# Kernel tuning notes

Measured on AMD Instinct MI355X. Metric: run time of the kernel, lower is better.

The kernel has to match this reference:

```python
import jax, jax.numpy as jnp
import numpy as np

B, D, H, E, K = 8192, 1024, 4096, 8, 2
LOSS_COEF = 0.01
EPS_COMBINE = float(np.finfo(np.float64).eps)  # np.finfo(float).eps used in combine


def setup_inputs() -> dict:
    key = jax.random.key(0)
    ks = jax.random.split(key, 6)
    s_in = 1.0 / np.sqrt(D)
    s_hid = 1.0 / np.sqrt(H)
    return {
        "x": jax.random.normal(ks[0], (B, D), jnp.float32),
        "w_gate": jax.random.uniform(ks[1], (E, D), jnp.float32, -s_in, s_in),
        "fc1_w": jax.random.uniform(ks[2], (E, H, D), jnp.float32, -s_in, s_in),
        "fc1_b": jax.random.uniform(ks[3], (E, H), jnp.float32, -s_in, s_in),
        "fc2_w": jax.random.uniform(ks[4], (E, D, H), jnp.float32, -s_hid, s_hid),
        "fc2_b": jax.random.uniform(ks[5], (E, D), jnp.float32, -s_hid, s_hid),
    }


def _cv_squared(v):
    # torch .var() uses ddof=1
    return jnp.var(v, ddof=1) / (jnp.mean(v) ** 2 + 1e-10)


def _top_k_gating(x, w_gate):
    # clean logits (noisy_gating=False): [B, E]
    logits = x @ w_gate.T
    top_vals, top_idx = jax.lax.top_k(logits, K + 1)  # min(k+1, E)
    topk_vals = top_vals[:, :K]
    topk_idx = top_idx[:, :K]
    topk_gates = jax.nn.softmax(topk_vals, axis=1)
    gates = jnp.zeros((x.shape[0], E), x.dtype)
    gates = gates.at[jnp.arange(x.shape[0])[:, None], topk_idx].set(topk_gates)
    return gates


def _forward(x, w_gate, fc1_w, fc1_b, fc2_w, fc2_b):
    gates = _top_k_gating(x, w_gate)            # [B, E], sparse (k nonzeros/row)
    importance = gates.sum(axis=0)              # [E]
    load = (gates > 0).sum(axis=0).astype(jnp.float32)
    loss = (_cv_squared(importance) + _cv_squared(load)) * LOSS_COEF

    # Dense-equivalent expert compute: tokens with gate==0 contribute 0 to the
    # combine, identical math to SparseDispatcher's gather/scatter.
    h = jnp.einsum('bd,ehd->beh', x, fc1_w) + fc1_b            # [B, E, H]
    h = jax.nn.gelu(h, approximate=False)                      # torch exact gelu
    o = jnp.einsum('beh,edh->bed', h, fc2_w) + fc2_b           # [B, E, D]
    log_p = jax.nn.log_softmax(o, axis=-1)                     # LogSoftmax(dim=1)

    # combine: exp, weight by gates, scatter-add, eps-fill, log
    combined = jnp.einsum('be,bed->bd', gates, jnp.exp(log_p)) # [B, D]
    combined = jnp.where(combined == 0, EPS_COMBINE, combined)
    y = jnp.log(combined)
    return y, loss


def reference(x, w_gate, fc1_w, fc1_b, fc2_w, fc2_b):
    return _forward(x, w_gate, fc1_w, fc1_b, fc2_w, fc2_b)
```

## Files before the change

### kernel.cpp

```cpp
#include <hip/hip_runtime.h>
#include <cstdint>
#include <cmath>

#define BT 8192
#define DD 1024
#define HH 4096
#define EE 8
#define MT2 72

typedef __attribute__((ext_vector_type(8))) short short8;
typedef __attribute__((ext_vector_type(4))) float f32x4;
typedef unsigned short u16;
typedef unsigned int u32;

__device__ __forceinline__ u16 f2bf(float f) {
    u32 u = __float_as_uint(f);
    u += 0x7FFFu + ((u >> 16) & 1u);
    return (u16)(u >> 16);
}

__device__ __forceinline__ void gld_lds16(const void* g, void* l) {
    __builtin_amdgcn_global_load_lds((__attribute__((address_space(1))) void*)g,
                                     (__attribute__((address_space(3))) void*)l,
                                     16, 0, 0);
}

__global__ void cvt_kernel(const float* __restrict__ src, u16* __restrict__ dst, int n8) {
    int i = blockIdx.x * blockDim.x + threadIdx.x;
    if (i >= n8) return;
    size_t base = (size_t)i * 8;
    float4 a = *(const float4*)(src + base);
    float4 b = *(const float4*)(src + base + 4);
    uint4 o;
    o.x = (u32)f2bf(a.x) | ((u32)f2bf(a.y) << 16);
    o.y = (u32)f2bf(a.z) | ((u32)f2bf(a.w) << 16);
    o.z = (u32)f2bf(b.x) | ((u32)f2bf(b.y) << 16);
    o.w = (u32)f2bf(b.z) | ((u32)f2bf(b.w) << 16);
    *(uint4*)(dst + base) = o;
}

__global__ void gating_kernel(const float* __restrict__ x, const float* __restrict__ wg,
                              float* __restrict__ gate_arr, int* __restrict__ list,
                              int* __restrict__ info,
                              int* __restrict__ counts, float* __restrict__ importance) {
    int wave = (blockIdx.x * blockDim.x + threadIdx.x) >> 6;
    int lane = threadIdx.x & 63;
    if (wave >= BT) return;
    const float* xr = x + (size_t)wave * DD;
    double acc[EE];
#pragma unroll
    for (int e = 0; e < EE; ++e) acc[e] = 0.0;
#pragma unroll
    for (int c = 0; c < DD / 256; ++c) {
        const int i = c * 256 + lane * 4;
        float4 xv = *(const float4*)(xr + i);
        double x0 = xv.x, x1 = xv.y, x2 = xv.z, x3 = xv.w;
#pragma unroll
        for (int e = 0; e < EE; ++e) {
            float4 wv = *(const float4*)(wg + e * DD + i);
            acc[e] += x0 * (double)wv.x + x1 * (double)wv.y
                    + x2 * (double)wv.z + x3 * (double)wv.w;
        }
    }
#pragma unroll
    for (int e = 0; e < EE; ++e) {
        double v = acc[e];
        for (int off = 32; off; off >>= 1) v += __shfl_down(v, off, 64);
        acc[e] = v;
    }
    if (lane == 0) {
        int i0 = 0; double v0 = acc[0];
        for (int e = 1; e < EE; ++e) if (acc[e] > v0) { v0 = acc[e]; i0 = e; }
        int i1 = -1; double v1 = -1e300;
        for (int e = 0; e < EE; ++e) { if (e == i0) continue; if (acc[e] > v1) { v1 = acc[e]; i1 = e; } }
        double e1 = exp(v1 - v0);
        double s = 1.0 + e1;
        float g0 = (float)(1.0 / s);
        float g1 = (float)(e1 / s);
        gate_arr[2 * wave]     = g0;
        gate_arr[2 * wave + 1] = g1;
        atomicAdd(&importance[i0], g0);
        atomicAdd(&importance[i1], g1);
        int p0 = atomicAdd(&counts[i0], 1);
        list[i0 * BT + p0] = wave;
        int p1 = atomicAdd(&counts[i1], 1);
        list[i1 * BT + p1] = wave;
        info[2 * wave]     = (i0 << 16) | p0;
        info[2 * wave + 1] = (i1 << 16) | p1;
    }
}

__global__ void loss_kernel(const int* __restrict__ counts, const float* __restrict__ importance,
                            int* __restrict__ offs, float* __restrict__ out_loss,
                            int* __restrict__ tmap, int* __restrict__ ntiles) {
    if (threadIdx.x == 0 && blockIdx.x == 0) {
        double mi = 0, ml = 0;
        int off = 0;
        for (int e = 0; e < EE; e++) {
            offs[e] = off; off += counts[e];
            mi += (double)importance[e]; ml += (double)counts[e];
        }
        mi /= EE; ml /= EE;
        double vi = 0, vl = 0;
        for (int e = 0; e < EE; e++) {
            double di = (double)importance[e] - mi; vi += di * di;
            double dl = (double)counts[e] - ml;     vl += dl * dl;
        }
        vi /= (EE - 1); vl /= (EE - 1);
        double cv_i = vi / (mi * mi + 1e-10);
        double cv_l = vl / (ml * ml + 1e-10);
        *out_loss = (float)((cv_i + cv_l) * 0.01);
        int ntl = 0;
        for (int e = 0; e < EE; e++)
            for (int t = 0; t < counts[e]; t += 256)
                tmap[ntl++] = (e << 20) | t;
        *ntiles = ntl;
    }
}

__global__ void gather_x_kernel(const float* __restrict__ x, const int* __restrict__ list,
                                const int* __restrict__ counts, const int* __restrict__ offs,
                                u16* __restrict__ xg) {
    int r = blockIdx.x;
    int e = 0;
#pragma unroll
    for (int i = 1; i < EE; ++i) if (r >= offs[i]) e = i;
    int m = r - offs[e];
    if (m >= counts[e]) return;
    int token = list[e * BT + m];
    const float* src = x + (size_t)token * DD;
    u16* dst = xg + (size_t)r * DD;
    int i = threadIdx.x * 4;
    float4 a = *(const float4*)(src + i);
    uint2 o;
    o.x = (u32)f2bf(a.x) | ((u32)f2bf(a.y) << 16);
    o.y = (u32)f2bf(a.z) | ((u32)f2bf(a.w) << 16);
    *(uint2*)(dst + i) = o;
}

template <int K, int NT, bool GELU, bool GATHER>
__global__ __launch_bounds__(512) void moe_gemm(const u16* __restrict__ Asrc,
                                                const u16* __restrict__ Bsrc,
                                                const float* __restrict__ bias,
                                                const int* __restrict__ list,
                                                const int* __restrict__ counts,
                                                const int* __restrict__ offs,
                                                const int* __restrict__ tmap,
                                                const int* __restrict__ ntiles,
                                                u16* __restrict__ outB,
                                                float* __restrict__ outF) {
    constexpr int NXT = NT / 256;
    constexpr int nwg = NXT * MT2;
    constexpr int QW = nwg / 8;
    constexpr int ITERS = K / 128;
    const int tid = threadIdx.x;
    const int lane = tid & 63;
    const int wv = tid >> 6;
    const int wqr = wv >> 2;
    const int wqc = wv & 3;
    const int kq = lane >> 4;
    const int rsub = lane & 15;
    const int rq = kq * 4;
    const int ks1 = tid >> 7;
    const int r128 = tid & 127;

    __shared__ u16 Ls[2][2][2][8192];

    const int nw = *ntiles;

#define STAGE_A(db, h, T)                                                   \
    do {                                                                    \
        gld_lds16(aP##h + (T) * 64,      &Ls[db][0][h][tid * 8]);           \
        gld_lds16(aP##h + (T) * 64 + 32, &Ls[db][0][h][(tid + 512) * 8]);   \
    } while (0)
#define STAGE_B(db, h, T)                                                   \
    do {                                                                    \
        gld_lds16(bP##h + (T) * 64,      &Ls[db][1][h][tid * 8]);           \
        gld_lds16(bP##h + (T) * 64 + 32, &Ls[db][1][h][(tid + 512) * 8]);   \
    } while (0)
#define WAIT4 asm volatile("s_waitcnt vmcnt(4)" ::: "memory")
#define WAIT0 asm volatile("s_waitcnt vmcnt(0)" ::: "memory")
#define NOOP ((void)0)

#define PH(db, mh, nh, RDA, STG, WT)                                          \
    do {                                                                      \
        if (RDA) {                                                            \
            _Pragma("unroll") for (int kk = 0; kk < 2; kk++)                  \
            _Pragma("unroll") for (int mi = 0; mi < 4; mi++)                  \
                afr[mi][kk] = *(const short8*)&Ls[db][0][mh]                  \
                    [((kk * 4 + kq) * 128 + wqr * 64 + mi * 16 + rsub) * 8];  \
        }                                                                     \
        _Pragma("unroll") for (int kk = 0; kk < 2; kk++)                      \
        _Pragma("unroll") for (int ni = 0; ni < 2; ni++)                      \
            bfr[ni][kk] = *(const short8*)&Ls[db][1][nh]                      \
                [((kk * 4 + kq) * 128 + wqc * 32 + ni * 16 + rsub) * 8];      \
        STG;                                                                  \
        __builtin_amdgcn_s_barrier();                                         \
        __builtin_amdgcn_s_setprio(1);                                        \
        _Pragma("unroll") for (int mi = 0; mi < 4; mi++)                      \
        _Pragma("unroll") for (int ni = 0; ni < 2; ni++)                      \
        _Pragma("unroll") for (int kk = 0; kk < 2; kk++)                      \
            acc[mh][nh][mi][ni] = __builtin_amdgcn_mfma_f32_16x16x32_bf16(    \
                afr[mi][kk], bfr[ni][kk], acc[mh][nh][mi][ni], 0, 0, 0);      \
        __builtin_amdgcn_s_setprio(0);                                        \
        WT;                                                                   \
        __builtin_amdgcn_s_barrier();                                         \
    } while (0)

#pragma unroll 1
    for (int raw = blockIdx.x; raw < nwg; raw += 256) {
        const int wg = (raw & 7) * QW + (raw >> 3);
        const int nt = wg / MT2;
        const int mt = wg - nt * MT2;
        if (mt >= nw) continue;
        const int ent = tmap[mt];
        const int e = ent >> 20;
        const int mbase = ent & 0xFFFFF;
        const int mmax = counts[e] - mbase;
        const int rowbase = offs[e] + mbase;
        const int nbase = nt * 256;

        size_t arow0, arow1;
        if constexpr (GATHER) {
            arow0 = (size_t)list[e * BT + mbase + min(r128, mmax - 1)];
            arow1 = (size_t)list[e * BT + mbase + min(128 + r128, mmax - 1)];
        } else {
            arow0 = (size_t)(rowbase + min(r128, mmax - 1));
            arow1 = (size_t)(rowbase + min(128 + r128, mmax - 1));
        }
        const u16* aP0 = Asrc + arow0 * (size_t)K + ks1 * 8;
        const u16* aP1 = Asrc + arow1 * (size_t)K + ks1 * 8;
        const u16* bP0 = Bsrc + ((size_t)e * NT + nbase + r128) * (size_t)K + ks1 * 8;
        const u16* bP1 = bP0 + (size_t)128 * K;

        f32x4 acc[2][2][4][2] = {};
        short8 afr[4][2], bfr[2][2];

        STAGE_A(0, 0, 0); STAGE_B(0, 0, 0); STAGE_A(0, 1, 0); STAGE_B(0, 1, 0);
        STAGE_A(1, 0, 1); STAGE_B(1, 0, 1);
        WAIT4;
        __builtin_amdgcn_s_barrier();

#pragma unroll 1
        for (int it = 0; it < ITERS - 1; ++it) {
            const int t = 2 * it;
            PH(0, 0, 0, 1, STAGE_A(1, 1, t + 1), NOOP);
            PH(0, 0, 1, 0, STAGE_B(1, 1, t + 1), NOOP);
            PH(0, 1, 0, 1, STAGE_A(0, 0, t + 2), NOOP);
            PH(0, 1, 1, 0, STAGE_B(0, 0, t + 2), WAIT4);
            PH(1, 0, 0, 1, STAGE_A(0, 1, t + 2), NOOP);
            PH(1, 0, 1, 0, STAGE_B(0, 1, t + 2), NOOP);
            PH(1, 1, 0, 1, STAGE_A(1, 0, t + 3), NOOP);
            PH(1, 1, 1, 0, STAGE_B(1, 0, t + 3), WAIT4);
        }
        {
            const int t = 2 * (ITERS - 1);
            PH(0, 0, 0, 1, STAGE_A(1, 1, t + 1), NOOP);
            PH(0, 0, 1, 0, STAGE_B(1, 1, t + 1), NOOP);
            PH(0, 1, 0, 1, NOOP, NOOP);
            PH(0, 1, 1, 0, NOOP, WAIT0);
            PH(1, 0, 0, 1, NOOP, NOOP);
            PH(1, 0, 1, 0, NOOP, NOOP);
            PH(1, 1, 0, 1, NOOP, NOOP);
            PH(1, 1, 1, 0, NOOP, NOOP);
        }

        float bvals[2][2];
#pragma unroll
        for (int nh = 0; nh < 2; nh++)
#pragma unroll
            for (int ni = 0; ni < 2; ni++)
                bvals[nh][ni] = bias[(size_t)e * NT + nbase + nh * 128 + wqc * 32 + ni * 16 + rsub];
#pragma unroll
        for (int mh = 0; mh < 2; mh++) {
#pragma unroll
            for (int mi = 0; mi < 4; mi++) {
#pragma unroll
                for (int r = 0; r < 4; r++) {
                    int m = mh * 128 + wqr * 64 + mi * 16 + rq + r;
                    if (m < mmax) {
                        size_t ro = (size_t)(rowbase + m);
#pragma unroll
                        for (int nh = 0; nh < 2; nh++) {
#pragma unroll
                            for (int ni = 0; ni < 2; ni++) {
                                int n = nbase + nh * 128 + wqc * 32 + ni * 16 + rsub;
                                float v = acc[mh][nh][mi][ni][r] + bvals[nh][ni];
                                if constexpr (GELU) {
                                    v = 0.5f * v * (1.0f + erff(v * 0.7071067811865476f));
                                    outB[ro * NT + n] = f2bf(v);
                                } else {
                                    outF[ro * NT + n] = v;
                                }
                            }
                        }
                    }
                }
            }
        }
        WAIT0;
    }
#undef PH
#undef STAGE_A
#undef STAGE_B
#undef WAIT4
#undef WAIT0
#undef NOOP
}

__global__ void combine_kernel(const float* __restrict__ o, const float* __restrict__ gates,
                               const int* __restrict__ info, const int* __restrict__ offs,
                               float* __restrict__ y) {
    const int b = blockIdx.x;
    const int tid = threadIdx.x;
    const int lane = tid & 63, wv = tid >> 6;
    const int inf0 = info[2 * b], inf1 = info[2 * b + 1];
    const int r0i = offs[inf0 >> 16] + (inf0 & 0xffff);
    const int r1i = offs[inf1 >> 16] + (inf1 & 0xffff);
    const float* r0 = o + (size_t)r0i * DD;
    const float* r1 = o + (size_t)r1i * DD;
    float v0[4], v1[4];
#pragma unroll
    for (int j = 0; j < 4; j++) { v0[j] = r0[tid + 256 * j]; v1[j] = r1[tid + 256 * j]; }
    float m0 = fmaxf(fmaxf(v0[0], v0[1]), fmaxf(v0[2], v0[3]));
    float m1 = fmaxf(fmaxf(v1[0], v1[1]), fmaxf(v1[2], v1[3]));
#pragma unroll
    for (int off = 32; off; off >>= 1) {
        m0 = fmaxf(m0, __shfl_xor(m0, off, 64));
        m1 = fmaxf(m1, __shfl_xor(m1, off, 64));
    }
    __shared__ float sred[2][4];
    if (lane == 0) { sred[0][wv] = m0; sred[1][wv] = m1; }
    __syncthreads();
    m0 = fmaxf(fmaxf(sred[0][0], sred[0][1]), fmaxf(sred[0][2], sred[0][3]));
    m1 = fmaxf(fmaxf(sred[1][0], sred[1][1]), fmaxf(sred[1][2], sred[1][3]));
    float p0[4], p1[4], s0 = 0.f, s1 = 0.f;
#pragma unroll
    for (int j = 0; j < 4; j++) {
        p0[j] = expf(v0[j] - m0); s0 += p0[j];
        p1[j] = expf(v1[j] - m1); s1 += p1[j];
    }
#pragma unroll
    for (int off = 32; off; off >>= 1) {
        s0 += __shfl_xor(s0, off, 64);
        s1 += __shfl_xor(s1, off, 64);
    }
    __shared__ float sred2[2][4];
    if (lane == 0) { sred2[0][wv] = s0; sred2[1][wv] = s1; }
    __syncthreads();
    s0 = sred2[0][0] + sred2[0][1] + sred2[0][2] + sred2[0][3];
    s1 = sred2[1][0] + sred2[1][1] + sred2[1][2] + sred2[1][3];
    const float c0 = gates[2 * b] / s0;
    const float c1 = gates[2 * b + 1] / s1;
#pragma unroll
    for (int j = 0; j < 4; j++) {
        float c = p0[j] * c0 + p1[j] * c1;
        if (c == 0.f) c = 2.2204460492503131e-16f;
        y[(size_t)b * DD + tid + 256 * j] = logf(c);
    }
}

extern "C" void kernel_launch(void* const* d_in, const int* in_sizes, int n_in,
                              void* d_out, int out_size, void* d_ws, size_t ws_size,
                              hipStream_t stream) {
    const float* x     = (const float*)d_in[0];
    const float* wgate = (const float*)d_in[1];
    const float* fc1w  = (const float*)d_in[2];
    const float* fc1b  = (const float*)d_in[3];
    const float* fc2w  = (const float*)d_in[4];
    const float* fc2b  = (const float*)d_in[5];
    float* out = (float*)d_out;

    char* ws = (char*)d_ws;
    const size_t MB = 1024 * 1024;
    const bool big = ws_size >= 289 * MB;
    u16* w1b = (u16*)(ws);
    float* o = (float*)(ws);
    u16* w2b = (u16*)(ws + 64 * MB);
    u16* xb  = (u16*)(ws + 128 * MB);
    u16* h   = (u16*)(ws + (big ? 128 : 144) * MB);
    u16* xg  = (u16*)(ws + 256 * MB);
    char* meta = ws + (big ? 288 : 272) * MB;
    int* counts       = (int*)meta;
    int* offs         = (int*)(meta + 32);
    float* importance = (float*)(meta + 64);
    int* ntiles       = (int*)(meta + 96);
    float* gate_arr   = (float*)(meta + 128);
    int* info         = (int*)(meta + 128 + 65536);
    int* list         = (int*)(meta + 128 + 131072);
    int* tmap         = (int*)(meta + 512 * 1024);

    hipMemsetAsync(meta, 0, 96, stream);
    cvt_kernel<<<(EE * HH * DD / 8 + 255) / 256, 256, 0, stream>>>(fc1w, w1b, EE * HH * DD / 8);
    cvt_kernel<<<(EE * DD * HH / 8 + 255) / 256, 256, 0, stream>>>(fc2w, w2b, EE * DD * HH / 8);
    gating_kernel<<<BT / 4, 256, 0, stream>>>(x, wgate, gate_arr, list, info, counts, importance);
    loss_kernel<<<1, 64, 0, stream>>>(counts, importance, offs, out + (size_t)BT * DD, tmap, ntiles);

    if (big) {
        gather_x_kernel<<<2 * BT, 256, 0, stream>>>(x, list, counts, offs, xg);
        moe_gemm<DD, HH, true, false><<<256, 512, 0, stream>>>(
            xg, w1b, fc1b, nullptr, counts, offs, tmap, ntiles, h, nullptr);
    } else {
        cvt_kernel<<<(BT * DD / 8 + 255) / 256, 256, 0, stream>>>(x, xb, BT * DD / 8);
        moe_gemm<DD, HH, true, true><<<256, 512, 0, stream>>>(
            xb, w1b, fc1b, list, counts, offs, tmap, ntiles, h, nullptr);
    }
    moe_gemm<HH, DD, false, false><<<256, 512, 0, stream>>>(
        h, w2b, fc2b, nullptr, counts, offs, tmap, ntiles, nullptr, o);
    combine_kernel<<<BT, 256, 0, stream>>>(o, gate_arr, info, offs, out);
}
```

Baseline: 1.150 ms.

## Software-pipeline LDS fragment reads one phase ahead of MFMA in grouped GEMM

Restructures the GEMM main loop so A/B fragment reads from LDS are double-buffered in registers and issued one phase ahead of the MFMA block that consumes them. Each phase now has one barrier instead of two, and the wait depth changes from vmcnt(4) to vmcnt(2), with extra barriers around the waits. The aim is to hide LDS read latency behind matrix-core work and cut barrier count. In exchange it needs more fragment registers, which could reduce occupancy, and the changed buffer-reuse ordering risks races if a read overlaps a stage write.

```diff
diff --git a/kernel.cpp b/kernel.cpp
--- a/kernel.cpp
+++ b/kernel.cpp
@@ -179,32 +179,33 @@
         gld_lds16(bP##h + (T) * 64 + 32, &Ls[db][1][h][(tid + 512) * 8]);   \
     } while (0)
 #define WAIT4 asm volatile("s_waitcnt vmcnt(4)" ::: "memory")
+#define WAIT2 asm volatile("s_waitcnt vmcnt(2)" ::: "memory")
 #define WAIT0 asm volatile("s_waitcnt vmcnt(0)" ::: "memory")
-#define NOOP ((void)0)
-
-#define PH(db, mh, nh, RDA, STG, WT)                                          \
+#define BAR __builtin_amdgcn_s_barrier()
+
+#define READ_A(s, db, mh)                                                     \
     do {                                                                      \
-        if (RDA) {                                                            \
-            _Pragma("unroll") for (int kk = 0; kk < 2; kk++)                  \
-            _Pragma("unroll") for (int mi = 0; mi < 4; mi++)                  \
-                afr[mi][kk] = *(const short8*)&Ls[db][0][mh]                  \
-                    [((kk * 4 + kq) * 128 + wqr * 64 + mi * 16 + rsub) * 8];  \
-        }                                                                     \
+        _Pragma("unroll") for (int kk = 0; kk < 2; kk++)                      \
+        _Pragma("unroll") for (int mi = 0; mi < 4; mi++)                      \
+            afr[s][mi][kk] = *(const short8*)&Ls[db][0][mh]                   \
+                [((kk * 4 + kq) * 128 + wqr * 64 + mi * 16 + rsub) * 8];      \
+    } while (0)
+#define READ_B(nh, db)                                                        \
+    do {                                                                      \
         _Pragma("unroll") for (int kk = 0; kk < 2; kk++)                      \
         _Pragma("unroll") for (int ni = 0; ni < 2; ni++)                      \
-            bfr[ni][kk] = *(const short8*)&Ls[db][1][nh]                      \
+            bfr[nh][ni][kk] = *(const short8*)&Ls[db][1][nh]                  \
                 [((kk * 4 + kq) * 128 + wqc * 32 + ni * 16 + rsub) * 8];      \
-        STG;                                                                  \
-        __builtin_amdgcn_s_barrier();                                         \
+    } while (0)
+#define MFMAQ(s, mh, nh)                                                      \
+    do {                                                                      \
         __builtin_amdgcn_s_setprio(1);                                        \
         _Pragma("unroll") for (int mi = 0; mi < 4; mi++)                      \
         _Pragma("unroll") for (int ni = 0; ni < 2; ni++)                      \
         _Pragma("unroll") for (int kk = 0; kk < 2; kk++)                      \
             acc[mh][nh][mi][ni] = __builtin_amdgcn_mfma_f32_16x16x32_bf16(    \
-                afr[mi][kk], bfr[ni][kk], acc[mh][nh][mi][ni], 0, 0, 0);      \
+                afr[s][mi][kk], bfr[nh][ni][kk], acc[mh][nh][mi][ni], 0, 0, 0);\
         __builtin_amdgcn_s_setprio(0);                                        \
-        WT;                                                                   \
-        __builtin_amdgcn_s_barrier();                                         \
     } while (0)
 
 #pragma unroll 1
@@ -234,35 +235,44 @@
         const u16* bP1 = bP0 + (size_t)128 * K;
 
         f32x4 acc[2][2][4][2] = {};
-        short8 afr[4][2], bfr[2][2];
+        short8 afr[2][4][2];
+        short8 bfr[2][2][2];
 
         STAGE_A(0, 0, 0); STAGE_B(0, 0, 0); STAGE_A(0, 1, 0); STAGE_B(0, 1, 0);
         STAGE_A(1, 0, 1); STAGE_B(1, 0, 1);
         WAIT4;
-        __builtin_amdgcn_s_barrier();
+        BAR;
+        READ_A(0, 0, 0);
+        READ_B(0, 0);
 
 #pragma unroll 1
         for (int it = 0; it < ITERS - 1; ++it) {
             const int t = 2 * it;
-            PH(0, 0, 0, 1, STAGE_A(1, 1, t + 1), NOOP);
-            PH(0, 0, 1, 0, STAGE_B(1, 1, t + 1), NOOP);
-            PH(0, 1, 0, 1, STAGE_A(0, 0, t + 2), NOOP);
-            PH(0, 1, 1, 0, STAGE_B(0, 0, t + 2), WAIT4);
-            PH(1, 0, 0, 1, STAGE_A(0, 1, t + 2), NOOP);
-            PH(1, 0, 1, 0, STAGE_B(0, 1, t + 2), NOOP);
-            PH(1, 1, 0, 1, STAGE_A(1, 0, t + 3), NOOP);
-            PH(1, 1, 1, 0, STAGE_B(1, 0, t + 3), WAIT4);
+            READ_B(1, 0);  STAGE_A(1, 1, t + 1);  MFMAQ(0, 0, 0);  BAR;
+            READ_A(1, 0, 1);  STAGE_B(1, 1, t + 1);  MFMAQ(0, 0, 1);  BAR;
+            STAGE_A(0, 0, t + 2);  MFMAQ(1, 1, 0);  BAR;
+            WAIT2;  BAR;
+            READ_A(0, 1, 0);  READ_B(0, 1);
+            STAGE_B(0, 0, t + 2);  MFMAQ(1, 1, 1);  BAR;
+            READ_B(1, 1);  STAGE_A(0, 1, t + 2);  MFMAQ(0, 0, 0);  BAR;
+            READ_A(1, 1, 1);  STAGE_B(0, 1, t + 2);  MFMAQ(0, 0, 1);  BAR;
+            STAGE_A(1, 0, t + 3);  MFMAQ(1, 1, 0);  BAR;
+            WAIT2;  BAR;
+            READ_A(0, 0, 0);  READ_B(0, 0);
+            STAGE_B(1, 0, t + 3);  MFMAQ(1, 1, 1);  BAR;
         }
         {
             const int t = 2 * (ITERS - 1);
-            PH(0, 0, 0, 1, STAGE_A(1, 1, t + 1), NOOP);
-            PH(0, 0, 1, 0, STAGE_B(1, 1, t + 1), NOOP);
-            PH(0, 1, 0, 1, NOOP, NOOP);
-            PH(0, 1, 1, 0, NOOP, WAIT0);
-            PH(1, 0, 0, 1, NOOP, NOOP);
-            PH(1, 0, 1, 0, NOOP, NOOP);
-            PH(1, 1, 0, 1, NOOP, NOOP);
-            PH(1, 1, 1, 0, NOOP, NOOP);
+            READ_B(1, 0);  STAGE_A(1, 1, t + 1);  MFMAQ(0, 0, 0);  BAR;
+            READ_A(1, 0, 1);  STAGE_B(1, 1, t + 1);  MFMAQ(0, 0, 1);  BAR;
+            MFMAQ(1, 1, 0);  BAR;
+            WAIT0;  BAR;
+            READ_A(0, 1, 0);  READ_B(0, 1);
+            MFMAQ(1, 1, 1);  BAR;
+            READ_B(1, 1);  MFMAQ(0, 0, 0);  BAR;
+            READ_A(1, 1, 1);  MFMAQ(0, 0, 1);  BAR;
+            MFMAQ(1, 1, 0);  BAR;
+            MFMAQ(1, 1, 1);  BAR;
         }
 
         float bvals[2][2];
@@ -300,12 +310,15 @@
         }
         WAIT0;
     }
-#undef PH
+#undef READ_A
+#undef READ_B
+#undef MFMAQ
 #undef STAGE_A
 #undef STAGE_B
 #undef WAIT4
+#undef WAIT2
 #undef WAIT0
-#undef NOOP
+#undef BAR
 }
 
 __global__ void combine_kernel(const float* __restrict__ o, const float* __restrict__ gates,
```

After: 1.914 ms. 66.4% more time.
